# Kernel optimization log

Measured on AMD Instinct MI355X. Metric: run time of the kernel, lower is better.

## Reference

```python
import jax, jax.numpy as jnp
import numpy as np

NEG_BIG = -9e15
ALPHA = 0.2  # LeakyReLU negative slope


def setup_inputs() -> dict:
    key = jax.random.key(0)
    k1, k2, k3, k4 = jax.random.split(key, 4)
    B, N, Fin, Fout = 4, 2048, 128, 128
    h = jax.random.normal(k1, (B, N, Fin), dtype=jnp.float32)
    adj = jax.random.randint(k2, (N, N), 0, 2, dtype=jnp.int32)
    W = jax.random.normal(k3, (Fin, Fout), dtype=jnp.float32) * 0.1
    a = jax.random.normal(k4, (2 * Fout, 1), dtype=jnp.float32) * 0.1
    return {"h": h, "adj": adj, "W": W, "a": a}


def reference(h, adj, W, a):
    # Wh: [B, N, Fout]
    Wh = jnp.einsum('bnf,fo->bno', h, W)
    Fout = W.shape[1]
    a1 = a[:Fout, 0]   # attends to source i
    a2 = a[Fout:, 0]   # attends to target j
    # Decomposed form of leakyrelu(cat([Wh_i, Wh_j]) @ a):
    # e_ij = leakyrelu(a1.Wh_i + a2.Wh_j)  -> [B, N, N]
    f1 = Wh @ a1  # [B, N]
    f2 = Wh @ a2  # [B, N]
    e = jax.nn.leaky_relu(f1[:, :, None] + f2[:, None, :], negative_slope=ALPHA)
    attention = jnp.where(adj[None, :, :] > 0, e, jnp.float32(NEG_BIG))
    attention = jax.nn.softmax(attention, axis=2)
    # dropout is identity in eval mode
    h_prime = jnp.einsum('bij,bjo->bio', attention, Wh)
    return h_prime
```

## Files before the change

### kernel.cpp

```cpp
#include <hip/hip_runtime.h>

#define BB 4
#define NN 2048
#define FF 128
#define NP 2176
#define ALPHA 0.2f
#define SHIFT_C 16.0f

typedef short bf16x8 __attribute__((ext_vector_type(8)));
typedef float f32x4 __attribute__((ext_vector_type(4)));
typedef unsigned u32;

__device__ inline short f2bf(float f) {
    union { float f; unsigned u; } v; v.f = f;
    unsigned r = (v.u + 0x7FFFu + ((v.u >> 16) & 1u)) >> 16;
    return (short)r;
}
__device__ inline float bf2f(short s) {
    union { float f; unsigned u; } v;
    v.u = ((unsigned)(unsigned short)s) << 16;
    return v.f;
}

__device__ inline void cp16(const void* g, void* l) {
    __builtin_amdgcn_global_load_lds(
        (const __attribute__((address_space(1))) u32*)g,
        (__attribute__((address_space(3))) u32*)l, 16, 0, 0);
}

__global__ __launch_bounds__(256) void k_wh(const float* __restrict__ h,
                                            const float* __restrict__ W,
                                            const float* __restrict__ a,
                                            const int* __restrict__ adj,
                                            short* __restrict__ WhHiT,
                                            short* __restrict__ WhLoT,
                                            float* __restrict__ f1,
                                            float* __restrict__ f2,
                                            u32* __restrict__ adjp) {
    __shared__ float Wa[2 * FF];
    __shared__ float hs[16 * 128];
    int tid = threadIdx.x;
    int r0 = blockIdx.x * 16;

    {
        int fin = tid & 127;
        const float* av = (tid < 128) ? a : (a + FF);
        const float* wr = W + (size_t)fin * FF;
        float s = 0.f;
        for (int o = 0; o < FF; o += 4) {
            float4 wv = *(const float4*)(wr + o);
            float4 avv = *(const float4*)(av + o);
            s += wv.x * avv.x + wv.y * avv.y + wv.z * avv.z + wv.w * avv.w;
        }
        Wa[(tid < 128 ? 0 : FF) + fin] = s;
    }
    {
        const float4* src = (const float4*)(h + (size_t)r0 * FF);
        float4* dst = (float4*)hs;
        dst[tid] = src[tid];
        dst[256 + tid] = src[256 + tid];
    }
    {
        int w = tid >> 6, lane = tid & 63;
        int row = blockIdx.x * 4 + w;
        const int* ar = adj + (size_t)row * NN;
        for (int it = 0; it < 32; ++it) {
            int v = ar[it * 64 + lane];
            unsigned long long mask = __ballot(v > 0);
            if (lane == 0) adjp[row * 64 + it * 2] = (u32)mask;
            if (lane == 1) adjp[row * 64 + it * 2 + 1] = (u32)(mask >> 32);
        }
    }
    __syncthreads();

    {
        int w = tid >> 6, lane = tid & 63;
        float wa1_0 = Wa[lane], wa1_1 = Wa[lane + 64];
        float wa2_0 = Wa[FF + lane], wa2_1 = Wa[FF + lane + 64];
        for (int rr = 0; rr < 4; ++rr) {
            int rloc = w * 4 + rr;
            int row = r0 + rloc;
            float x0 = hs[rloc * FF + lane], x1 = hs[rloc * FF + lane + 64];
            float s1 = x0 * wa1_0 + x1 * wa1_1;
            float s2 = x0 * wa2_0 + x1 * wa2_1;
#pragma unroll
            for (int m = 32; m >= 1; m >>= 1) {
                s1 += __shfl_xor(s1, m, 64);
                s2 += __shfl_xor(s2, m, 64);
            }
            if (lane == 0) { f1[row] = s1; f2[row] = s2; }
        }
    }

    int f4 = (tid & 31) * 4;
    int rg = tid >> 5;
    float acc[2][4];
#pragma unroll
    for (int rr = 0; rr < 2; ++rr)
#pragma unroll
        for (int cc = 0; cc < 4; ++cc) acc[rr][cc] = 0.f;

    for (int k0 = 0; k0 < FF; k0 += 4) {
        float4 wv[4];
#pragma unroll
        for (int kk = 0; kk < 4; ++kk)
            wv[kk] = *(const float4*)(W + (size_t)(k0 + kk) * FF + f4);
        float4 hv[2];
#pragma unroll
        for (int rr = 0; rr < 2; ++rr)
            hv[rr] = *(const float4*)(hs + (rg * 2 + rr) * FF + k0);
#pragma unroll
        for (int rr = 0; rr < 2; ++rr) {
            float hk[4] = {hv[rr].x, hv[rr].y, hv[rr].z, hv[rr].w};
#pragma unroll
            for (int kk = 0; kk < 4; ++kk) {
                acc[rr][0] += hk[kk] * wv[kk].x;
                acc[rr][1] += hk[kk] * wv[kk].y;
                acc[rr][2] += hk[kk] * wv[kk].z;
                acc[rr][3] += hk[kk] * wv[kk].w;
            }
        }
    }
    int rloc = r0 + rg * 2;
    int b = rloc >> 11;
    int j = rloc & (NN - 1);
#pragma unroll
    for (int cc = 0; cc < 4; ++cc) {
        float v0 = acc[0][cc], v1 = acc[1][cc];
        short h0 = f2bf(v0), h1 = f2bf(v1);
        short l0 = f2bf(v0 - bf2f(h0)), l1 = f2bf(v1 - bf2f(h1));
        size_t off = (size_t)(b * FF + f4 + cc) * NP + j;
        *(short2*)(WhHiT + off) = make_short2(h0, h1);
        *(short2*)(WhLoT + off) = make_short2(l0, l1);
    }
}

__global__ __launch_bounds__(1024, 4) void k_attn(const short* __restrict__ WhHiT,
                                                  const short* __restrict__ WhLoT,
                                                  const u32* __restrict__ adjp,
                                                  const float* __restrict__ f1,
                                                  const float* __restrict__ f2,
                                                  float* __restrict__ out) {
    __shared__ __align__(16) char lds[55424];
    char* Bbuf = lds;
    char* A0 = lds + 49152;
    float* row_ps = (float*)(lds + 54272);
    float* row_inv = (float*)(lds + 55296);

    int tid = threadIdx.x;
    int w = tid >> 6, lane = tid & 63;
    int blk = blockIdx.x;
    int b = blk >> 6;
    int i0 = (blk & 63) * 32;

    int r_a = lane & 15, kg = lane >> 4;
    int mi = w >> 3, ni = w & 7;

    int rb = tid & 31;
    int jp = (tid >> 5) & 15;
    bool abuild = tid < 512;
    float f1i = abuild ? f1[b * NN + i0 + rb] : 0.f;
    const u32* aprow = adjp + (size_t)(i0 + rb) * 64;
    const float* f2b = f2 + b * NN;
    int aoff = (rb >> 4) * 1280 + (rb & 15) * 80 + jp * 4;

    int hw = w & 7;
    int isLo = w >> 3;
    int fo_s = hw * 16 + (lane >> 2);
    int oc_s = lane & 3;
    const short* gB = (isLo ? WhLoT : WhHiT) + (size_t)(b * FF + fo_s) * NP + oc_s * 8;
    int bB = isLo * 8192 + hw * 1024;

    f32x4 acc = {0.f, 0.f, 0.f, 0.f};
    float sp = 0.f;

    cp16(gB, Bbuf + bB);
    float2 pf2 = {0.f, 0.f};
    u32 pmw = 0;
    if (abuild) {
        float2 q = *(const float2*)(f2b + jp * 2);
        u32 mw = aprow[0];
        float x0 = f1i + q.x, x1 = f1i + q.y;
        x0 = fmaxf(x0, ALPHA * x0);
        x1 = fmaxf(x1, ALPHA * x1);
        float p0 = __expf(x0 - SHIFT_C) * (float)((mw >> (jp * 2)) & 1u);
        float p1 = __expf(x1 - SHIFT_C) * (float)((mw >> (jp * 2 + 1)) & 1u);
        sp += p0 + p1;
        union { float f; u32 u; } u0, u1; u0.f = p0; u1.f = p1;
        *(u32*)(A0 + aoff) = ((u0.u + 0x8000u) >> 16) | (((u1.u + 0x8000u) >> 16) << 16);
        pf2 = *(const float2*)(f2b + 32 + jp * 2);
        pmw = aprow[1];
    }
    __syncthreads();

    int cur = 0, nxt = 1;
    for (int s = 0; s < 64; ++s) {
        {
            int jn = ((s + 1) & 63) * 32;
            cp16(gB + jn, Bbuf + nxt * 16384 + bB);
        }
        if (abuild) {
            char* wa = A0 + ((s + 1) & 1) * 2560;
            float x0 = f1i + pf2.x, x1 = f1i + pf2.y;
            x0 = fmaxf(x0, ALPHA * x0);
            x1 = fmaxf(x1, ALPHA * x1);
            float p0 = __expf(x0 - SHIFT_C) * (float)((pmw >> (jp * 2)) & 1u);
            float p1 = __expf(x1 - SHIFT_C) * (float)((pmw >> (jp * 2 + 1)) & 1u);
            if (s < 63) sp += p0 + p1;
            union { float f; u32 u; } u0, u1; u0.f = p0; u1.f = p1;
            *(u32*)(wa + aoff) = ((u0.u + 0x8000u) >> 16) | (((u1.u + 0x8000u) >> 16) << 16);
            int sn = (s + 2) & 63;
            pf2 = *(const float2*)(f2b + sn * 32 + jp * 2);
            pmw = aprow[sn];
        }
        {
            char* rbuf = Bbuf + cur * 16384;
            char* abuf = A0 + (s & 1) * 2560;
            bf16x8 af = *(const bf16x8*)(abuf + mi * 1280 + r_a * 80 + kg * 16);
            const char* p = rbuf + ((ni * 16 + r_a) * 64 + kg * 16);
            bf16x8 bh = *(const bf16x8*)p;
            bf16x8 bl = *(const bf16x8*)(p + 8192);
            acc = __builtin_amdgcn_mfma_f32_16x16x32_bf16(af, bh, acc, 0, 0, 0);
            acc = __builtin_amdgcn_mfma_f32_16x16x32_bf16(af, bl, acc, 0, 0, 0);
        }
        __syncthreads();
        cur = nxt;
        nxt = (nxt == 2) ? 0 : nxt + 1;
    }

    sp += __shfl_xor(sp, 32, 64);
    if (w < 8 && lane < 32) row_ps[w * 32 + lane] = sp;
    __syncthreads();
    if (tid < 32) {
        float t = 0.f;
#pragma unroll
        for (int ww = 0; ww < 8; ++ww) t += row_ps[ww * 32 + tid];
        row_inv[tid] = 1.0f / t;
    }
    __syncthreads();

    float* ob = out + ((size_t)b * NN + i0 + mi * 16) * FF + ni * 16;
#pragma unroll
    for (int q = 0; q < 4; ++q) {
        int rr = kg * 4 + q;
        ob[(size_t)rr * FF + r_a] = acc[q] * row_inv[mi * 16 + rr];
    }
}

extern "C" void kernel_launch(void* const* d_in, const int* in_sizes, int n_in,
                              void* d_out, int out_size, void* d_ws, size_t ws_size,
                              hipStream_t stream) {
    const float* h   = (const float*)d_in[0];
    const int*   adj = (const int*)d_in[1];
    const float* W   = (const float*)d_in[2];
    const float* a   = (const float*)d_in[3];
    float* out = (float*)d_out;

    short* WhHiT = (short*)d_ws;
    short* WhLoT = WhHiT + (size_t)BB * FF * NP;
    float* f1 = (float*)(WhLoT + (size_t)BB * FF * NP);
    float* f2 = f1 + (size_t)BB * NN;
    u32* adjp = (u32*)(f2 + (size_t)BB * NN);

    k_wh<<<(BB * NN) / 16, 256, 0, stream>>>(h, W, a, adj, WhHiT, WhLoT, f1, f2, adjp);
    k_attn<<<BB * (NN / 32), 1024, 0, stream>>>(WhHiT, WhLoT, adjp, f1, f2, out);
}
```

Measured before the change: 149.1 us.

## Split attention blocks across output-feature halves and process two K-chunks per barrier

The attention kernel now launches 512 blocks of 512 threads. Each block covers 32 rows and one half of the output features, so the grid is twice as large. Each loop iteration stages two 32-wide K chunks, double-buffered, which halves the number of block barriers. The softmax probability tile is now recomputed redundantly by both feature-half blocks. Separately, adjacency bit-packing now uses per-thread int4 loads that build a 32-bit word directly, replacing the wave ballot loop.

```diff
diff --git a/kernel.cpp b/kernel.cpp
--- a/kernel.cpp
+++ b/kernel.cpp
@@ -61,15 +61,19 @@
         dst[256 + tid] = src[256 + tid];
     }
     {
-        int w = tid >> 6, lane = tid & 63;
-        int row = blockIdx.x * 4 + w;
-        const int* ar = adj + (size_t)row * NN;
-        for (int it = 0; it < 32; ++it) {
-            int v = ar[it * 64 + lane];
-            unsigned long long mask = __ballot(v > 0);
-            if (lane == 0) adjp[row * 64 + it * 2] = (u32)mask;
-            if (lane == 1) adjp[row * 64 + it * 2 + 1] = (u32)(mask >> 32);
-        }
+        int g = blockIdx.x * 256 + tid;
+        int row = g >> 6, wd = g & 63;
+        const int4* ar = (const int4*)(adj + (size_t)row * NN + wd * 32);
+        u32 word = 0;
+#pragma unroll
+        for (int q = 0; q < 8; ++q) {
+            int4 v = ar[q];
+            word |= (u32)(v.x > 0) << (q * 4);
+            word |= (u32)(v.y > 0) << (q * 4 + 1);
+            word |= (u32)(v.z > 0) << (q * 4 + 2);
+            word |= (u32)(v.w > 0) << (q * 4 + 3);
+        }
+        adjp[row * 64 + wd] = word;
     }
     __syncthreads();
 
@@ -135,101 +139,126 @@
     }
 }
 
-__global__ __launch_bounds__(1024, 4) void k_attn(const short* __restrict__ WhHiT,
-                                                  const short* __restrict__ WhLoT,
-                                                  const u32* __restrict__ adjp,
-                                                  const float* __restrict__ f1,
-                                                  const float* __restrict__ f2,
-                                                  float* __restrict__ out) {
-    __shared__ __align__(16) char lds[55424];
-    char* Bbuf = lds;
-    char* A0 = lds + 49152;
-    float* row_ps = (float*)(lds + 54272);
-    float* row_inv = (float*)(lds + 55296);
+__global__ __launch_bounds__(512, 4) void k_attn(const short* __restrict__ WhHiT,
+                                                 const short* __restrict__ WhLoT,
+                                                 const u32* __restrict__ adjp,
+                                                 const float* __restrict__ f1,
+                                                 const float* __restrict__ f2,
+                                                 float* __restrict__ out) {
+    __shared__ __align__(16) char lds[44160];
+    char* Bb = lds;
+    char* Ab = lds + 32768;
+    float* row_ps = (float*)(lds + 43008);
+    float* row_inv = (float*)(lds + 44032);
 
     int tid = threadIdx.x;
     int w = tid >> 6, lane = tid & 63;
     int blk = blockIdx.x;
-    int b = blk >> 6;
-    int i0 = (blk & 63) * 32;
+    int b = blk >> 7;
+    int tile = (blk >> 1) & 63;
+    int half = blk & 1;
+    int i0 = tile * 32;
 
     int r_a = lane & 15, kg = lane >> 4;
-    int mi = w >> 3, ni = w & 7;
+    int mi = w >> 2, ni = w & 3;
 
     int rb = tid & 31;
     int jp = (tid >> 5) & 15;
-    bool abuild = tid < 512;
-    float f1i = abuild ? f1[b * NN + i0 + rb] : 0.f;
+    float f1i = f1[b * NN + i0 + rb];
     const u32* aprow = adjp + (size_t)(i0 + rb) * 64;
     const float* f2b = f2 + b * NN;
     int aoff = (rb >> 4) * 1280 + (rb & 15) * 80 + jp * 4;
 
-    int hw = w & 7;
-    int isLo = w >> 3;
-    int fo_s = hw * 16 + (lane >> 2);
+    int isLo = w >> 2;
+    int sub = w & 3;
+    int fo_s = half * 64 + sub * 16 + (lane >> 2);
     int oc_s = lane & 3;
     const short* gB = (isLo ? WhLoT : WhHiT) + (size_t)(b * FF + fo_s) * NP + oc_s * 8;
-    int bB = isLo * 8192 + hw * 1024;
+    int bB = isLo * 4096 + sub * 1024;
 
     f32x4 acc = {0.f, 0.f, 0.f, 0.f};
     float sp = 0.f;
 
-    cp16(gB, Bbuf + bB);
-    float2 pf2 = {0.f, 0.f};
-    u32 pmw = 0;
-    if (abuild) {
-        float2 q = *(const float2*)(f2b + jp * 2);
-        u32 mw = aprow[0];
-        float x0 = f1i + q.x, x1 = f1i + q.y;
-        x0 = fmaxf(x0, ALPHA * x0);
-        x1 = fmaxf(x1, ALPHA * x1);
-        float p0 = __expf(x0 - SHIFT_C) * (float)((mw >> (jp * 2)) & 1u);
-        float p1 = __expf(x1 - SHIFT_C) * (float)((mw >> (jp * 2 + 1)) & 1u);
-        sp += p0 + p1;
-        union { float f; u32 u; } u0, u1; u0.f = p0; u1.f = p1;
-        *(u32*)(A0 + aoff) = ((u0.u + 0x8000u) >> 16) | (((u1.u + 0x8000u) >> 16) << 16);
-        pf2 = *(const float2*)(f2b + 32 + jp * 2);
-        pmw = aprow[1];
-    }
-    __syncthreads();
-
-    int cur = 0, nxt = 1;
-    for (int s = 0; s < 64; ++s) {
-        {
-            int jn = ((s + 1) & 63) * 32;
-            cp16(gB + jn, Bbuf + nxt * 16384 + bB);
-        }
-        if (abuild) {
-            char* wa = A0 + ((s + 1) & 1) * 2560;
-            float x0 = f1i + pf2.x, x1 = f1i + pf2.y;
-            x0 = fmaxf(x0, ALPHA * x0);
-            x1 = fmaxf(x1, ALPHA * x1);
-            float p0 = __expf(x0 - SHIFT_C) * (float)((pmw >> (jp * 2)) & 1u);
-            float p1 = __expf(x1 - SHIFT_C) * (float)((pmw >> (jp * 2 + 1)) & 1u);
-            if (s < 63) sp += p0 + p1;
-            union { float f; u32 u; } u0, u1; u0.f = p0; u1.f = p1;
-            *(u32*)(wa + aoff) = ((u0.u + 0x8000u) >> 16) | (((u1.u + 0x8000u) >> 16) << 16);
-            int sn = (s + 2) & 63;
-            pf2 = *(const float2*)(f2b + sn * 32 + jp * 2);
-            pmw = aprow[sn];
-        }
-        {
-            char* rbuf = Bbuf + cur * 16384;
-            char* abuf = A0 + (s & 1) * 2560;
-            bf16x8 af = *(const bf16x8*)(abuf + mi * 1280 + r_a * 80 + kg * 16);
-            const char* p = rbuf + ((ni * 16 + r_a) * 64 + kg * 16);
-            bf16x8 bh = *(const bf16x8*)p;
-            bf16x8 bl = *(const bf16x8*)(p + 8192);
-            acc = __builtin_amdgcn_mfma_f32_16x16x32_bf16(af, bh, acc, 0, 0, 0);
-            acc = __builtin_amdgcn_mfma_f32_16x16x32_bf16(af, bl, acc, 0, 0, 0);
+    cp16(gB, Bb + bB);
+    cp16(gB + 32, Bb + 8192 + bB);
+    {
+        float2 qa = *(const float2*)(f2b + jp * 2);
+        float2 qb = *(const float2*)(f2b + 32 + jp * 2);
+        u32 wa = aprow[0], wb = aprow[1];
+        float x;
+        x = f1i + qa.x; x = fmaxf(x, ALPHA * x);
+        float p00 = __expf(x - SHIFT_C) * (float)((wa >> (jp * 2)) & 1u);
+        x = f1i + qa.y; x = fmaxf(x, ALPHA * x);
+        float p01 = __expf(x - SHIFT_C) * (float)((wa >> (jp * 2 + 1)) & 1u);
+        x = f1i + qb.x; x = fmaxf(x, ALPHA * x);
+        float p10 = __expf(x - SHIFT_C) * (float)((wb >> (jp * 2)) & 1u);
+        x = f1i + qb.y; x = fmaxf(x, ALPHA * x);
+        float p11 = __expf(x - SHIFT_C) * (float)((wb >> (jp * 2 + 1)) & 1u);
+        sp += p00 + p01 + p10 + p11;
+        union { float f; u32 u; } u0, u1;
+        u0.f = p00; u1.f = p01;
+        *(u32*)(Ab + aoff) = ((u0.u + 0x8000u) >> 16) | (((u1.u + 0x8000u) >> 16) << 16);
+        u0.f = p10; u1.f = p11;
+        *(u32*)(Ab + 2560 + aoff) = ((u0.u + 0x8000u) >> 16) | (((u1.u + 0x8000u) >> 16) << 16);
+    }
+    float2 pfa = *(const float2*)(f2b + 64 + jp * 2);
+    float2 pfb = *(const float2*)(f2b + 96 + jp * 2);
+    u32 pwa = aprow[2], pwb = aprow[3];
+    __syncthreads();
+
+    for (int p = 0; p < 32; ++p) {
+        int par = p & 1, opar = par ^ 1;
+        {
+            int j0n = ((2 * p + 2) & 63) * 32;
+            int j1n = ((2 * p + 3) & 63) * 32;
+            cp16(gB + j0n, Bb + opar * 16384 + bB);
+            cp16(gB + j1n, Bb + opar * 16384 + 8192 + bB);
+        }
+        {
+            float x;
+            x = f1i + pfa.x; x = fmaxf(x, ALPHA * x);
+            float p00 = __expf(x - SHIFT_C) * (float)((pwa >> (jp * 2)) & 1u);
+            x = f1i + pfa.y; x = fmaxf(x, ALPHA * x);
+            float p01 = __expf(x - SHIFT_C) * (float)((pwa >> (jp * 2 + 1)) & 1u);
+            x = f1i + pfb.x; x = fmaxf(x, ALPHA * x);
+            float p10 = __expf(x - SHIFT_C) * (float)((pwb >> (jp * 2)) & 1u);
+            x = f1i + pfb.y; x = fmaxf(x, ALPHA * x);
+            float p11 = __expf(x - SHIFT_C) * (float)((pwb >> (jp * 2 + 1)) & 1u);
+            if (p < 31) sp += p00 + p01 + p10 + p11;
+            union { float f; u32 u; } u0, u1;
+            u0.f = p00; u1.f = p01;
+            *(u32*)(Ab + opar * 5120 + aoff) =
+                ((u0.u + 0x8000u) >> 16) | (((u1.u + 0x8000u) >> 16) << 16);
+            u0.f = p10; u1.f = p11;
+            *(u32*)(Ab + opar * 5120 + 2560 + aoff) =
+                ((u0.u + 0x8000u) >> 16) | (((u1.u + 0x8000u) >> 16) << 16);
+        }
+        {
+            int s0 = (2 * p + 4) & 63, s1 = (2 * p + 5) & 63;
+            pfa = *(const float2*)(f2b + s0 * 32 + jp * 2);
+            pfb = *(const float2*)(f2b + s1 * 32 + jp * 2);
+            pwa = aprow[s0]; pwb = aprow[s1];
+        }
+        {
+            char* bbase = Bb + par * 16384;
+            char* abase = Ab + par * 5120;
+            int boff = (ni * 16 + r_a) * 64 + kg * 16;
+            bf16x8 af0 = *(const bf16x8*)(abase + mi * 1280 + r_a * 80 + kg * 16);
+            bf16x8 b0h = *(const bf16x8*)(bbase + boff);
+            bf16x8 b0l = *(const bf16x8*)(bbase + 4096 + boff);
+            acc = __builtin_amdgcn_mfma_f32_16x16x32_bf16(af0, b0h, acc, 0, 0, 0);
+            acc = __builtin_amdgcn_mfma_f32_16x16x32_bf16(af0, b0l, acc, 0, 0, 0);
+            bf16x8 af1 = *(const bf16x8*)(abase + 2560 + mi * 1280 + r_a * 80 + kg * 16);
+            bf16x8 b1h = *(const bf16x8*)(bbase + 8192 + boff);
+            bf16x8 b1l = *(const bf16x8*)(bbase + 8192 + 4096 + boff);
+            acc = __builtin_amdgcn_mfma_f32_16x16x32_bf16(af1, b1h, acc, 0, 0, 0);
+            acc = __builtin_amdgcn_mfma_f32_16x16x32_bf16(af1, b1l, acc, 0, 0, 0);
         }
         __syncthreads();
-        cur = nxt;
-        nxt = (nxt == 2) ? 0 : nxt + 1;
     }
 
     sp += __shfl_xor(sp, 32, 64);
-    if (w < 8 && lane < 32) row_ps[w * 32 + lane] = sp;
+    if (lane < 32) row_ps[w * 32 + lane] = sp;
     __syncthreads();
     if (tid < 32) {
         float t = 0.f;
@@ -239,7 +268,7 @@
     }
     __syncthreads();
 
-    float* ob = out + ((size_t)b * NN + i0 + mi * 16) * FF + ni * 16;
+    float* ob = out + ((size_t)b * NN + i0 + mi * 16) * FF + half * 64 + ni * 16;
 #pragma unroll
     for (int q = 0; q < 4; ++q) {
         int rr = kg * 4 + q;
@@ -263,5 +292,5 @@
     u32* adjp = (u32*)(f2 + (size_t)BB * NN);
 
     k_wh<<<(BB * NN) / 16, 256, 0, stream>>>(h, W, a, adj, WhHiT, WhLoT, f1, f2, adjp);
-    k_attn<<<BB * (NN / 32), 1024, 0, stream>>>(WhHiT, WhLoT, adjp, f1, f2, out);
-}
+    k_attn<<<512, 512, 0, stream>>>(WhHiT, WhLoT, adjp, f1, f2, out);
+}
```

Measured after the change: 137.7 us. 7.6% less time.
